# Optimization experiments

Hardware: AMD Instinct MI355X
Metric: run time of the kernel (lower is better)

Reference implementation:

```python
import jax, jax.numpy as jnp
import numpy as np


def setup_inputs() -> dict:
    key = jax.random.key(0)
    k_u, k_ev, k_lam = jax.random.split(key, 3)
    B, K, L = 64, 32, 8192
    u = jax.random.normal(k_u, (B, L), dtype=jnp.float32)
    # synthetic stand-in for load_or_compute_eigen_data
    eigenvectors = jax.random.normal(k_ev, (K, L), dtype=jnp.float32)
    # module stores eigenvalues ** 0.25
    eigenvalues = jax.random.uniform(k_lam, (K,), dtype=jnp.float32) ** 0.25
    return {"u": u, "eigenvectors": eigenvectors, "eigenvalues": eigenvalues}


def reference(u, eigenvectors, eigenvalues):
    L = u.shape[-1]
    u_fft = jnp.fft.rfft(u)                    # (B, L//2+1) complex
    ev_fft = jnp.fft.rfft(eigenvectors)        # (K, L//2+1) complex (precomputed param in torch)
    # NOTE: faithful to torch einsum 'bi,kj->bkj' which SUMS over i
    p_fft = jnp.einsum('bi,kj->bkj', u_fft, ev_fft)   # (B, K, L//2+1)
    convolutions = jnp.fft.irfft(p_fft, n=L)           # (B, K, L)
    result = jnp.einsum('bkl,k->bl', convolutions, eigenvalues)  # (B, L)
    return result
```

## Files before the change

### kernel.cpp

```cpp
#include <hip/hip_runtime.h>
#include <math.h>

constexpr int Lc = 8192;
constexpr int Kc = 32;
constexpr int Bc = 64;
constexpr int NSLICE = 32;
constexpr int NCHUNK = 8;

__device__ inline float cot_pi_frac_f(int d) {
    int dd = d; float s = 1.0f;
    if (dd > Lc / 2) { dd = Lc - dd; s = -1.0f; }
    float ang = (float)(M_PI * (double)dd / (double)Lc);
    return s * __fdividef(__cosf(ang), __sinf(ang));
}


__global__ __launch_bounds__(256) void k_prep(
    const float* __restrict__ u, const float* __restrict__ ev,
    const float* __restrict__ lam, float* __restrict__ w,
    float* __restrict__ c, float* __restrict__ sr, float* __restrict__ si2)
{
    const int blk = blockIdx.x, t = threadIdx.x;
    if (blk < 32) {
        int n = blk * 256 + t;
        float acc = 0.f;
#pragma unroll
        for (int k = 0; k < Kc; ++k)
            acc = fmaf(lam[k], ev[k * Lc + n], acc);
        w[n] = acc;
    } else if (blk < 48) {
        int m = (blk - 32) * 256 + t;
        c[m] = cot_pi_frac_f(2 * m + 1);
    } else {
        int b = blk - 48;
        const float4* u4 = (const float4*)(u + (size_t)b * Lc);
        float ar0 = 0.f, ar1 = 0.f, ai0 = 0.f, ai1 = 0.f;
#pragma unroll
        for (int i = 0; i < 8; ++i) {
            int j = t + 256 * i;
            float4 v = u4[j];
            ar0 += v.x; ar1 += v.z;
            ai0 = fmaf(v.y, cot_pi_frac_f(4 * j + 1), ai0);
            ai1 = fmaf(v.w, cot_pi_frac_f(4 * j + 3), ai1);
        }
        if (t == 0) ar0 += 4096.0f * u[(size_t)b * Lc];
        float ar = ar0 + ar1, ai = ai0 + ai1;
        for (int off = 32; off > 0; off >>= 1) {
            ar += __shfl_down(ar, off);
            ai += __shfl_down(ai, off);
        }
        __shared__ float red[8];
        int wave = t >> 6, lane = t & 63;
        if (lane == 0) { red[wave] = ar; red[4 + wave] = ai; }
        __syncthreads();
        if (t == 0) {
            sr[b]  = red[0] + red[1] + red[2] + red[3];
            si2[b] = (2.0f / (float)Lc) * (red[4] + red[5] + red[6] + red[7]);
        }
    }
}

__global__ __launch_bounds__(256) void k_conv(
    const float* __restrict__ w, const float* __restrict__ c,
    float* __restrict__ Bp)
{
    __shared__ float s_we[641];
    __shared__ float s_wo[640];
    __shared__ float s_c[128];

    const int t  = threadIdx.x;
    const int cn = blockIdx.x & (NCHUNK - 1);
    const int sl = blockIdx.x >> 3;
    const int n0 = cn * 1024;
    const int dbase = sl * 256;
    const int wbase = n0 - dbase - 255;

    for (int j = t; j < 640; j += 256) {
        s_we[j] = w[(wbase + 2 * j + 2 * Lc) & (Lc - 1)];
        s_wo[j] = w[(wbase + 2 * j + 1 + 2 * Lc) & (Lc - 1)];
    }
    if (t < 128) s_c[t] = c[sl * 128 + 127 - t];
    __syncthreads();

    const int g = t >> 1, p = t & 1;
    const float* s_wp = p ? s_wo : s_we;
    const int jb = 4 * g;

    float W0 = s_wp[jb],     W1 = s_wp[jb + 1], W2 = s_wp[jb + 2], W3 = s_wp[jb + 3];
    float W4 = s_wp[jb + 4], W5 = s_wp[jb + 5], W6 = s_wp[jb + 6];
    float a0 = 0.f, a1 = 0.f, a2 = 0.f, a3 = 0.f;

#pragma unroll
    for (int G = 0; G < 32; ++G) {
        const int mm0 = 4 * G;
        float c0 = s_c[mm0], c1 = s_c[mm0 + 1], c2 = s_c[mm0 + 2], c3 = s_c[mm0 + 3];
        a0 = fmaf(c0, W0, a0); a1 = fmaf(c0, W1, a1); a2 = fmaf(c0, W2, a2); a3 = fmaf(c0, W3, a3);
        a0 = fmaf(c1, W1, a0); a1 = fmaf(c1, W2, a1); a2 = fmaf(c1, W3, a2); a3 = fmaf(c1, W4, a3);
        a0 = fmaf(c2, W2, a0); a1 = fmaf(c2, W3, a1); a2 = fmaf(c2, W4, a2); a3 = fmaf(c2, W5, a3);
        a0 = fmaf(c3, W3, a0); a1 = fmaf(c3, W4, a1); a2 = fmaf(c3, W5, a2); a3 = fmaf(c3, W6, a3);
        if (G < 31) {
            W0 = W4; W1 = W5; W2 = W6;
            W3 = s_wp[jb + mm0 + 7];  W4 = s_wp[jb + mm0 + 8];
            W5 = s_wp[jb + mm0 + 9];  W6 = s_wp[jb + mm0 + 10];
        }
    }
    float* dst = Bp + (size_t)sl * Lc + n0 + 8 * g + p;
    dst[0] = a0; dst[2] = a1; dst[4] = a2; dst[6] = a3;
}

__global__ __launch_bounds__(256) void k_out(
    const float* __restrict__ w, const float* __restrict__ sr,
    const float* __restrict__ si2, const float* __restrict__ Bp,
    float* __restrict__ out)
{
    __shared__ float s_sv[128];
    const int t = threadIdx.x;
    if (t < 128) s_sv[t] = (t < 64) ? sr[t] : si2[t - 64];
    const int cn = blockIdx.x & 31, bg = blockIdx.x >> 5;
    const int n = cn * 256 + t;
    float bsum = 0.f;
#pragma unroll
    for (int s = 0; s < NSLICE; ++s) bsum += Bp[(size_t)s * Lc + n];
    float wv = w[n];
    __syncthreads();
#pragma unroll
    for (int j = 0; j < 8; ++j) {
        int b = bg * 8 + j;
        out[(size_t)b * Lc + n] = fmaf(s_sv[b], wv, s_sv[64 + b] * bsum);
    }
}

extern "C" void kernel_launch(void* const* d_in, const int* in_sizes, int n_in,
                              void* d_out, int out_size, void* d_ws, size_t ws_size,
                              hipStream_t stream) {
    const float* u   = (const float*)d_in[0];
    const float* ev  = (const float*)d_in[1];
    const float* lam = (const float*)d_in[2];
    float* out = (float*)d_out;

    float* ws  = (float*)d_ws;
    float* w   = ws;
    float* c   = ws + 8192;
    float* sr  = ws + 12288;
    float* si2 = ws + 12352;
    float* Bp  = ws + 12416;

    hipLaunchKernelGGL(k_prep, dim3(112), dim3(256), 0, stream, u, ev, lam, w, c, sr, si2);
    hipLaunchKernelGGL(k_conv, dim3(NCHUNK * NSLICE), dim3(256), 0, stream, w, c, Bp);
    hipLaunchKernelGGL(k_out,  dim3(256), dim3(256), 0, stream, w, sr, si2, Bp, out);
}
```

Before: 65.95 us.

## Fuse prep into conv kernel, recompute weighted eigenvector sum per block

```diff
diff --git a/kernel.cpp b/kernel.cpp
--- a/kernel.cpp
+++ b/kernel.cpp
@@ -15,24 +15,15 @@
 }
 
 
-__global__ __launch_bounds__(256) void k_prep(
+__global__ __launch_bounds__(256) void k_main(
     const float* __restrict__ u, const float* __restrict__ ev,
-    const float* __restrict__ lam, float* __restrict__ w,
-    float* __restrict__ c, float* __restrict__ sr, float* __restrict__ si2)
+    const float* __restrict__ lam, float* __restrict__ sr,
+    float* __restrict__ si2, float* __restrict__ Bp)
 {
-    const int blk = blockIdx.x, t = threadIdx.x;
-    if (blk < 32) {
-        int n = blk * 256 + t;
-        float acc = 0.f;
-#pragma unroll
-        for (int k = 0; k < Kc; ++k)
-            acc = fmaf(lam[k], ev[k * Lc + n], acc);
-        w[n] = acc;
-    } else if (blk < 48) {
-        int m = (blk - 32) * 256 + t;
-        c[m] = cot_pi_frac_f(2 * m + 1);
-    } else {
-        int b = blk - 48;
+    const int t = threadIdx.x;
+
+    if (blockIdx.x < 64) {
+        int b = blockIdx.x;
         const float4* u4 = (const float4*)(u + (size_t)b * Lc);
         float ar0 = 0.f, ar1 = 0.f, ai0 = 0.f, ai1 = 0.f;
 #pragma unroll
@@ -57,47 +48,57 @@
             sr[b]  = red[0] + red[1] + red[2] + red[3];
             si2[b] = (2.0f / (float)Lc) * (red[4] + red[5] + red[6] + red[7]);
         }
+        return;
     }
-}
 
-__global__ __launch_bounds__(256) void k_conv(
-    const float* __restrict__ w, const float* __restrict__ c,
-    float* __restrict__ Bp)
-{
-    __shared__ float s_we[641];
-    __shared__ float s_wo[640];
-    __shared__ float s_c[128];
+    __shared__ float s_we[643];
+    __shared__ float s_wo[643];
+    __shared__ __align__(16) float s_c[128];
 
-    const int t  = threadIdx.x;
-    const int cn = blockIdx.x & (NCHUNK - 1);
-    const int sl = blockIdx.x >> 3;
+    const int blk = blockIdx.x - 64;
+    const int cn = blk & (NCHUNK - 1);
+    const int sl = blk >> 3;
     const int n0 = cn * 1024;
     const int dbase = sl * 256;
-    const int wbase = n0 - dbase - 255;
+    const int A = n0 - dbase - 256;
 
-    for (int j = t; j < 640; j += 256) {
-        s_we[j] = w[(wbase + 2 * j + 2 * Lc) & (Lc - 1)];
-        s_wo[j] = w[(wbase + 2 * j + 1 + 2 * Lc) & (Lc - 1)];
+#pragma unroll
+    for (int it = 0; it < 2; ++it) {
+        int gq = t + 256 * it;
+        if (gq < 320) {
+            int pos = (A + 4 * gq + 2 * Lc) & (Lc - 1);
+            float4 acc = make_float4(0.f, 0.f, 0.f, 0.f);
+#pragma unroll
+            for (int k = 0; k < Kc; ++k) {
+                float4 v = *(const float4*)(ev + (size_t)k * Lc + pos);
+                float lk = lam[k];
+                acc.x = fmaf(lk, v.x, acc.x); acc.y = fmaf(lk, v.y, acc.y);
+                acc.z = fmaf(lk, v.z, acc.z); acc.w = fmaf(lk, v.w, acc.w);
+            }
+            s_we[2 * gq]     = acc.x; s_wo[2 * gq]     = acc.y;
+            s_we[2 * gq + 1] = acc.z; s_wo[2 * gq + 1] = acc.w;
+        }
     }
-    if (t < 128) s_c[t] = c[sl * 128 + 127 - t];
+    if (t < 128) s_c[t] = cot_pi_frac_f(dbase + 255 - 2 * t);
     __syncthreads();
 
     const int g = t >> 1, p = t & 1;
-    const float* s_wp = p ? s_wo : s_we;
+    const float* s_wp = p ? (s_we + 1) : s_wo;
     const int jb = 4 * g;
 
     float W0 = s_wp[jb],     W1 = s_wp[jb + 1], W2 = s_wp[jb + 2], W3 = s_wp[jb + 3];
     float W4 = s_wp[jb + 4], W5 = s_wp[jb + 5], W6 = s_wp[jb + 6];
     float a0 = 0.f, a1 = 0.f, a2 = 0.f, a3 = 0.f;
 
+    const float4* s_c4 = (const float4*)s_c;
 #pragma unroll
     for (int G = 0; G < 32; ++G) {
         const int mm0 = 4 * G;
-        float c0 = s_c[mm0], c1 = s_c[mm0 + 1], c2 = s_c[mm0 + 2], c3 = s_c[mm0 + 3];
-        a0 = fmaf(c0, W0, a0); a1 = fmaf(c0, W1, a1); a2 = fmaf(c0, W2, a2); a3 = fmaf(c0, W3, a3);
-        a0 = fmaf(c1, W1, a0); a1 = fmaf(c1, W2, a1); a2 = fmaf(c1, W3, a2); a3 = fmaf(c1, W4, a3);
-        a0 = fmaf(c2, W2, a0); a1 = fmaf(c2, W3, a1); a2 = fmaf(c2, W4, a2); a3 = fmaf(c2, W5, a3);
-        a0 = fmaf(c3, W3, a0); a1 = fmaf(c3, W4, a1); a2 = fmaf(c3, W5, a2); a3 = fmaf(c3, W6, a3);
+        float4 cv = s_c4[G];
+        a0 = fmaf(cv.x, W0, a0); a1 = fmaf(cv.x, W1, a1); a2 = fmaf(cv.x, W2, a2); a3 = fmaf(cv.x, W3, a3);
+        a0 = fmaf(cv.y, W1, a0); a1 = fmaf(cv.y, W2, a1); a2 = fmaf(cv.y, W3, a2); a3 = fmaf(cv.y, W4, a3);
+        a0 = fmaf(cv.z, W2, a0); a1 = fmaf(cv.z, W3, a1); a2 = fmaf(cv.z, W4, a2); a3 = fmaf(cv.z, W5, a3);
+        a0 = fmaf(cv.w, W3, a0); a1 = fmaf(cv.w, W4, a1); a2 = fmaf(cv.w, W5, a2); a3 = fmaf(cv.w, W6, a3);
         if (G < 31) {
             W0 = W4; W1 = W5; W2 = W6;
             W3 = s_wp[jb + mm0 + 7];  W4 = s_wp[jb + mm0 + 8];
@@ -109,19 +110,22 @@
 }
 
 __global__ __launch_bounds__(256) void k_out(
-    const float* __restrict__ w, const float* __restrict__ sr,
-    const float* __restrict__ si2, const float* __restrict__ Bp,
-    float* __restrict__ out)
+    const float* __restrict__ ev, const float* __restrict__ lam,
+    const float* __restrict__ sr, const float* __restrict__ si2,
+    const float* __restrict__ Bp, float* __restrict__ out)
 {
     __shared__ float s_sv[128];
     const int t = threadIdx.x;
     if (t < 128) s_sv[t] = (t < 64) ? sr[t] : si2[t - 64];
     const int cn = blockIdx.x & 31, bg = blockIdx.x >> 5;
     const int n = cn * 256 + t;
+    float wv = 0.f;
+#pragma unroll
+    for (int k = 0; k < Kc; ++k)
+        wv = fmaf(lam[k], ev[(size_t)k * Lc + n], wv);
     float bsum = 0.f;
 #pragma unroll
     for (int s = 0; s < NSLICE; ++s) bsum += Bp[(size_t)s * Lc + n];
-    float wv = w[n];
     __syncthreads();
 #pragma unroll
     for (int j = 0; j < 8; ++j) {
@@ -139,13 +143,12 @@
     float* out = (float*)d_out;
 
     float* ws  = (float*)d_ws;
-    float* w   = ws;
-    float* c   = ws + 8192;
-    float* sr  = ws + 12288;
-    float* si2 = ws + 12352;
-    float* Bp  = ws + 12416;
+    float* sr  = ws;
+    float* si2 = ws + 64;
+    float* Bp  = ws + 128;
 
-    hipLaunchKernelGGL(k_prep, dim3(112), dim3(256), 0, stream, u, ev, lam, w, c, sr, si2);
-    hipLaunchKernelGGL(k_conv, dim3(NCHUNK * NSLICE), dim3(256), 0, stream, w, c, Bp);
-    hipLaunchKernelGGL(k_out,  dim3(256), dim3(256), 0, stream, w, sr, si2, Bp, out);
+    hipLaunchKernelGGL(k_main, dim3(64 + NCHUNK * NSLICE), dim3(256), 0, stream,
+                       u, ev, lam, sr, si2, Bp);
+    hipLaunchKernelGGL(k_out, dim3(256), dim3(256), 0, stream,
+                       ev, lam, sr, si2, Bp, out);
 }
```

Measured after the change: 65.66 us. About the same (-0.4%).
